# Kernel tuning notes

Measured on AMD Instinct MI355X. Metric: run time of the kernel, lower is better.

Reference implementation:

```python
import jax, jax.numpy as jnp
import numpy as np

B, L, C_IN = 32, 8192, 64
K, F = 3, 128


def setup_inputs() -> dict:
    key = jax.random.key(0)
    k1, k2 = jax.random.split(key)
    x = jax.random.normal(k1, (B, L, C_IN), dtype=jnp.float32)
    # glorot-ish scale for the conv kernel [k, C_in, F] (TF WIO layout)
    w = jax.random.normal(k2, (K, C_IN, F), dtype=jnp.float32) * (2.0 / (K * C_IN + F)) ** 0.5
    b = jnp.zeros((F,), dtype=jnp.float32)
    return {"x": x, "w": w, "b": b}


def reference(x, w, b):
    # Original: per-position matmul+trace == valid conv1d; then bias + relu.
    # x: [B, L, C_in], w: [K, C_in, F] -> out: [B, L-K+1, F]
    out = jax.lax.conv_general_dilated(
        x, w,
        window_strides=(1,),
        padding="VALID",
        dimension_numbers=("NWC", "WIO", "NWC"),
    )
    return jax.nn.relu(out + b)
```

## Files before the change

### kernel.cpp

```cpp
#include <hip/hip_runtime.h>
#include <hip/hip_bf16.h>

typedef __attribute__((ext_vector_type(8))) short short8;
typedef __attribute__((ext_vector_type(4))) float floatx4;

#define B_SZ   32
#define L_IN   8192
#define C_INCH 64
#define KW     3
#define F_OUT  128
#define L_OUT  (L_IN - KW + 1)
#define KDIM   (KW * C_INCH)

#define TILE_L  64
#define AROWS   (TILE_L + 2)
#define ASTRIDE 72
#define NGRID   (B_SZ * (L_IN / TILE_L))

#define WTAB_ELEMS (8 * 6 * 64)

__device__ __forceinline__ unsigned pk2(float a, float b) {
    __hip_bfloat162 h = __float22bfloat162_rn(make_float2(a, b));
    unsigned u;
    __builtin_memcpy(&u, &h, 4);
    return u;
}

__global__ __launch_bounds__(256) void w_prep(const float* __restrict__ w,
                                              short8* __restrict__ wtab) {
    int id = blockIdx.x * 256 + threadIdx.x;
    if (id >= WTAB_ELEMS) return;
    int lane = id & 63;
    int s    = (id >> 6) % 6;
    int nt   = id / 384;
    int nl = lane & 15, q = lane >> 4;
    const float* __restrict__ wf = w + nt * 16 + nl;
    float t[8];
#pragma unroll
    for (int j = 0; j < 8; ++j) t[j] = wf[(s * 32 + q * 8 + j) * F_OUT];
    union { unsigned u[4]; short8 v; } hb;
    hb.u[0] = pk2(t[0], t[1]);
    hb.u[1] = pk2(t[2], t[3]);
    hb.u[2] = pk2(t[4], t[5]);
    hb.u[3] = pk2(t[6], t[7]);
    wtab[id] = hb.v;
}

template <bool PREP>
__global__ __launch_bounds__(256, 4) void conv1d_mfma(const float* __restrict__ x,
                                                      const float* __restrict__ w,
                                                      const float* __restrict__ bias,
                                                      float* __restrict__ out,
                                                      const short8* __restrict__ wtab) {
    __shared__ short a_lds[AROWS * ASTRIDE];

    const int tid  = threadIdx.x;
    const int lane = tid & 63;
    const int wave = tid >> 6;
    const int q    = lane >> 4;
    const int nl   = lane & 15;

    const int g  = blockIdx.x;
    const int b  = g >> 7;
    const int l0 = (g & 127) * TILE_L;

    short8 bfrag[6][2];
    if (PREP) {
#pragma unroll
        for (int n = 0; n < 2; ++n)
#pragma unroll
            for (int s = 0; s < 6; ++s)
                bfrag[s][n] = wtab[(((wave * 2 + n) * 6 + s) << 6) + lane];
    } else {
#pragma unroll
        for (int n = 0; n < 2; ++n) {
            const int f = (wave * 2 + n) * 16 + nl;
            const float* __restrict__ wf = w + f;
#pragma unroll
            for (int s = 0; s < 6; ++s) {
                float t[8];
#pragma unroll
                for (int j = 0; j < 8; ++j)
                    t[j] = wf[(s * 32 + q * 8 + j) * F_OUT];
                union { unsigned u[4]; short8 v; } hb;
                hb.u[0] = pk2(t[0], t[1]);
                hb.u[1] = pk2(t[2], t[3]);
                hb.u[2] = pk2(t[4], t[5]);
                hb.u[3] = pk2(t[6], t[7]);
                bfrag[s][n] = hb.v;
            }
        }
    }

    float4 bv[2];
#pragma unroll
    for (int n = 0; n < 2; ++n)
        bv[n] = *(const float4*)(bias + (wave * 2 + n) * 16 + q * 4);

#pragma unroll
    for (int i = 0; i < 3; ++i) {
        int c = tid + 256 * i;
        if (c < AROWS * 8) {
            int p   = c >> 3;
            int col = (c & 7) * 8;
            int gl  = l0 + p;
            float4 v0, v1;
            if (gl < L_IN) {
                const float4* xp =
                    (const float4*)(x + ((size_t)b * L_IN + gl) * C_INCH + col);
                v0 = xp[0];
                v1 = xp[1];
            } else {
                v0 = make_float4(0.f, 0.f, 0.f, 0.f);
                v1 = v0;
            }
            union { unsigned u[4]; short8 v; } h;
            h.u[0] = pk2(v0.x, v0.y);
            h.u[1] = pk2(v0.z, v0.w);
            h.u[2] = pk2(v1.x, v1.y);
            h.u[3] = pk2(v1.z, v1.w);
            *(short8*)&a_lds[p * ASTRIDE + col] = h.v;
        }
    }
    __syncthreads();

    floatx4 acc[4][2];
#pragma unroll
    for (int m = 0; m < 4; ++m)
#pragma unroll
        for (int n = 0; n < 2; ++n) acc[m][n] = (floatx4){0.f, 0.f, 0.f, 0.f};

#pragma unroll
    for (int s = 0; s < 6; ++s) {
#pragma unroll
        for (int m = 0; m < 4; ++m) {
            short8 af = *(const short8*)&a_lds[(m * 16 + nl + (s >> 1)) * ASTRIDE
                                               + (s & 1) * 32 + q * 8];
#pragma unroll
            for (int n = 0; n < 2; ++n)
                acc[m][n] = __builtin_amdgcn_mfma_f32_16x16x32_bf16(
                    bfrag[s][n], af, acc[m][n], 0, 0, 0);
        }
    }

#pragma unroll
    for (int n = 0; n < 2; ++n) {
        const int fb = (wave * 2 + n) * 16 + q * 4;
#pragma unroll
        for (int m = 0; m < 4; ++m) {
            const int l = l0 + m * 16 + nl;
            if (l < L_OUT) {
                float4 v;
                v.x = acc[m][n][0] + bv[n].x;
                v.y = acc[m][n][1] + bv[n].y;
                v.z = acc[m][n][2] + bv[n].z;
                v.w = acc[m][n][3] + bv[n].w;
                v.x = v.x > 0.f ? v.x : 0.f;
                v.y = v.y > 0.f ? v.y : 0.f;
                v.z = v.z > 0.f ? v.z : 0.f;
                v.w = v.w > 0.f ? v.w : 0.f;
                *(float4*)(out + ((size_t)b * L_OUT + l) * F_OUT + fb) = v;
            }
        }
    }
}

extern "C" void kernel_launch(void* const* d_in, const int* in_sizes, int n_in,
                              void* d_out, int out_size, void* d_ws, size_t ws_size,
                              hipStream_t stream) {
    const float* x    = (const float*)d_in[0];
    const float* w    = (const float*)d_in[1];
    const float* bias = (const float*)d_in[2];
    float* out        = (float*)d_out;

    if (d_ws != nullptr && ws_size >= (size_t)WTAB_ELEMS * sizeof(short8)) {
        short8* wtab = (short8*)d_ws;
        w_prep<<<dim3((WTAB_ELEMS + 255) / 256), 256, 0, stream>>>(w, wtab);
        conv1d_mfma<true><<<dim3(NGRID), 256, 0, stream>>>(x, w, bias, out, wtab);
    } else {
        conv1d_mfma<false><<<dim3(NGRID), 256, 0, stream>>>(x, w, bias, out, nullptr);
    }
}
```

Baseline: 191.7 us.

## Process four tiles per block with async global-to-LDS prefetch of next tile

Each block now handles four consecutive 64-row tiles, so the grid shrinks by a factor of four. The raw fp32 input is staged into LDS with global_load_lds. The next tile's load is issued before the current tile's MFMA and store phase, so input fetch overlaps compute and output writes. A separate pass converts the staged fp32 data to bf16 in a second LDS buffer. This adds LDS footprint, hand-placed waitcnt/barrier synchronisation whose correctness depends on vmcnt ordering, and fewer blocks in flight.

```diff
diff --git a/kernel.cpp b/kernel.cpp
--- a/kernel.cpp
+++ b/kernel.cpp
@@ -15,7 +15,11 @@
 #define TILE_L  64
 #define AROWS   (TILE_L + 2)
 #define ASTRIDE 72
-#define NGRID   (B_SZ * (L_IN / TILE_L))
+#define TPB     4
+#define NGRID   (B_SZ * (L_IN / TILE_L) / TPB)
+
+#define XCHUNKS (AROWS * 16)
+#define BUNITS  (AROWS * 8)
 
 #define WTAB_ELEMS (8 * 6 * 64)
 
@@ -52,7 +56,8 @@
                                                       const float* __restrict__ bias,
                                                       float* __restrict__ out,
                                                       const short8* __restrict__ wtab) {
-    __shared__ short a_lds[AROWS * ASTRIDE];
+    __shared__ __align__(16) float a_raw[AROWS * C_INCH];
+    __shared__ __align__(16) short b_lds[AROWS * ASTRIDE];
 
     const int tid  = threadIdx.x;
     const int lane = tid & 63;
@@ -60,9 +65,9 @@
     const int q    = lane >> 4;
     const int nl   = lane & 15;
 
-    const int g  = blockIdx.x;
-    const int b  = g >> 7;
-    const int l0 = (g & 127) * TILE_L;
+    const int g      = blockIdx.x;
+    const int b      = g >> 5;
+    const int l_base = (g & 31) * (TPB * TILE_L);
 
     short8 bfrag[6][2];
     if (PREP) {
@@ -97,70 +102,98 @@
     for (int n = 0; n < 2; ++n)
         bv[n] = *(const float4*)(bias + (wave * 2 + n) * 16 + q * 4);
 
-#pragma unroll
-    for (int i = 0; i < 3; ++i) {
-        int c = tid + 256 * i;
-        if (c < AROWS * 8) {
-            int p   = c >> 3;
-            int col = (c & 7) * 8;
-            int gl  = l0 + p;
-            float4 v0, v1;
-            if (gl < L_IN) {
-                const float4* xp =
-                    (const float4*)(x + ((size_t)b * L_IN + gl) * C_INCH + col);
-                v0 = xp[0];
-                v1 = xp[1];
-            } else {
-                v0 = make_float4(0.f, 0.f, 0.f, 0.f);
-                v1 = v0;
-            }
-            union { unsigned u[4]; short8 v; } h;
-            h.u[0] = pk2(v0.x, v0.y);
-            h.u[1] = pk2(v0.z, v0.w);
-            h.u[2] = pk2(v1.x, v1.y);
-            h.u[3] = pk2(v1.z, v1.w);
-            *(short8*)&a_lds[p * ASTRIDE + col] = h.v;
-        }
-    }
+    auto stage = [&](int l0) {
+#pragma unroll
+        for (int r = 0; r < 5; ++r) {
+            int c = r * 256 + tid;
+            if (c < XCHUNKS) {
+                int row  = c >> 4;
+                int pc   = c & 15;
+                int grow = b * L_IN + l0 + row;
+                grow = grow < (B_SZ * L_IN - 1) ?
+                       grow : (B_SZ * L_IN - 1);
+                const float* src = x + (size_t)grow * C_INCH + pc * 4;
+                float* dst = &a_raw[(r * 256 + wave * 64) * 4];
+                __builtin_amdgcn_global_load_lds(
+                    (const __attribute__((address_space(1))) void*)src,
+                    (__attribute__((address_space(3))) void*)dst, 16, 0, 0);
+            }
+        }
+    };
+
+    stage(l_base);
     __syncthreads();
 
-    floatx4 acc[4][2];
-#pragma unroll
-    for (int m = 0; m < 4; ++m)
-#pragma unroll
-        for (int n = 0; n < 2; ++n) acc[m][n] = (floatx4){0.f, 0.f, 0.f, 0.f};
-
-#pragma unroll
-    for (int s = 0; s < 6; ++s) {
-#pragma unroll
-        for (int m = 0; m < 4; ++m) {
-            short8 af = *(const short8*)&a_lds[(m * 16 + nl + (s >> 1)) * ASTRIDE
-                                               + (s & 1) * 32 + q * 8];
-#pragma unroll
-            for (int n = 0; n < 2; ++n)
-                acc[m][n] = __builtin_amdgcn_mfma_f32_16x16x32_bf16(
-                    bfrag[s][n], af, acc[m][n], 0, 0, 0);
-        }
-    }
-
-#pragma unroll
-    for (int n = 0; n < 2; ++n) {
-        const int fb = (wave * 2 + n) * 16 + q * 4;
-#pragma unroll
-        for (int m = 0; m < 4; ++m) {
-            const int l = l0 + m * 16 + nl;
-            if (l < L_OUT) {
-                float4 v;
-                v.x = acc[m][n][0] + bv[n].x;
-                v.y = acc[m][n][1] + bv[n].y;
-                v.z = acc[m][n][2] + bv[n].z;
-                v.w = acc[m][n][3] + bv[n].w;
-                v.x = v.x > 0.f ? v.x : 0.f;
-                v.y = v.y > 0.f ? v.y : 0.f;
-                v.z = v.z > 0.f ? v.z : 0.f;
-                v.w = v.w > 0.f ? v.w : 0.f;
-                *(float4*)(out + ((size_t)b * L_OUT + l) * F_OUT + fb) = v;
-            }
+#pragma unroll
+    for (int t = 0; t < TPB; ++t) {
+        const int l0 = l_base + t * TILE_L;
+
+#pragma unroll
+        for (int r = 0; r < 3; ++r) {
+            int u = r * 256 + tid;
+            if (u < BUNITS) {
+                int p = u >> 3, cb = u & 7;
+                const floatx4* ap = (const floatx4*)&a_raw[p * C_INCH + cb * 8];
+                floatx4 a0 = ap[0], a1 = ap[1];
+                union { unsigned uu[4]; short8 v; } h;
+                h.uu[0] = pk2(a0[0], a0[1]);
+                h.uu[1] = pk2(a0[2], a0[3]);
+                h.uu[2] = pk2(a1[0], a1[1]);
+                h.uu[3] = pk2(a1[2], a1[3]);
+                *(short8*)&b_lds[p * ASTRIDE + cb * 8] = h.v;
+            }
+        }
+        asm volatile("s_waitcnt lgkmcnt(0)" ::: "memory");
+        __builtin_amdgcn_s_barrier();
+
+        if (t + 1 < TPB) {
+            stage(l0 + TILE_L);
+            __builtin_amdgcn_sched_barrier(0);
+        }
+
+        floatx4 acc[4][2];
+#pragma unroll
+        for (int m = 0; m < 4; ++m)
+#pragma unroll
+            for (int n = 0; n < 2; ++n) acc[m][n] = (floatx4){0.f, 0.f, 0.f, 0.f};
+
+#pragma unroll
+        for (int s = 0; s < 6; ++s) {
+#pragma unroll
+            for (int m = 0; m < 4; ++m) {
+                short8 af = *(const short8*)&b_lds[(m * 16 + nl + (s >> 1)) * ASTRIDE
+                                                   + (s & 1) * 32 + q * 8];
+#pragma unroll
+                for (int n = 0; n < 2; ++n)
+                    acc[m][n] = __builtin_amdgcn_mfma_f32_16x16x32_bf16(
+                        bfrag[s][n], af, acc[m][n], 0, 0, 0);
+            }
+        }
+
+#pragma unroll
+        for (int n = 0; n < 2; ++n) {
+            const int fb = (wave * 2 + n) * 16 + q * 4;
+#pragma unroll
+            for (int m = 0; m < 4; ++m) {
+                const int l = l0 + m * 16 + nl;
+                if (l < L_OUT) {
+                    float4 v;
+                    v.x = acc[m][n][0] + bv[n].x;
+                    v.y = acc[m][n][1] + bv[n].y;
+                    v.z = acc[m][n][2] + bv[n].z;
+                    v.w = acc[m][n][3] + bv[n].w;
+                    v.x = v.x > 0.f ? v.x : 0.f;
+                    v.y = v.y > 0.f ? v.y : 0.f;
+                    v.z = v.z > 0.f ? v.z : 0.f;
+                    v.w = v.w > 0.f ? v.w : 0.f;
+                    *(float4*)(out + ((size_t)b * L_OUT + l) * F_OUT + fb) = v;
+                }
+            }
+        }
+
+        if (t + 1 < TPB) {
+            asm volatile("s_waitcnt vmcnt(8)" ::: "memory");
+            __builtin_amdgcn_s_barrier();
         }
     }
 }
```

New measurement: 204.3 us. 1.07x slower.

## Load x tile directly to LDS as fp32 with XOR swizzle, convert at read

Applied to the files above, without the earlier changes.

The input tile is now copied from global memory straight into LDS with global_load_lds in fp32, skipping the register round-trip and the bf16 packing at load time. A per-row XOR swizzle on 16-byte chunks is meant to avoid LDS bank conflicts on the fragment reads. The bf16 conversion moves into the MFMA loop, so each element gets converted several times (rows are reused across the three taps). LDS use roughly doubles, which may limit occupancy, and out-of-range rows are clamped rather than zeroed.

```diff
diff --git a/kernel.cpp b/kernel.cpp
--- a/kernel.cpp
+++ b/kernel.cpp
@@ -14,8 +14,9 @@
 
 #define TILE_L  64
 #define AROWS   (TILE_L + 2)
-#define ASTRIDE 72
 #define NGRID   (B_SZ * (L_IN / TILE_L))
+
+#define XCHUNKS (AROWS * 16)
 
 #define WTAB_ELEMS (8 * 6 * 64)
 
@@ -52,7 +53,7 @@
                                                       const float* __restrict__ bias,
                                                       float* __restrict__ out,
                                                       const short8* __restrict__ wtab) {
-    __shared__ short a_lds[AROWS * ASTRIDE];
+    __shared__ __align__(16) float a_raw[AROWS * C_INCH];
 
     const int tid  = threadIdx.x;
     const int lane = tid & 63;
@@ -98,28 +99,20 @@
         bv[n] = *(const float4*)(bias + (wave * 2 + n) * 16 + q * 4);
 
 #pragma unroll
-    for (int i = 0; i < 3; ++i) {
-        int c = tid + 256 * i;
-        if (c < AROWS * 8) {
-            int p   = c >> 3;
-            int col = (c & 7) * 8;
-            int gl  = l0 + p;
-            float4 v0, v1;
-            if (gl < L_IN) {
-                const float4* xp =
-                    (const float4*)(x + ((size_t)b * L_IN + gl) * C_INCH + col);
-                v0 = xp[0];
-                v1 = xp[1];
-            } else {
-                v0 = make_float4(0.f, 0.f, 0.f, 0.f);
-                v1 = v0;
-            }
-            union { unsigned u[4]; short8 v; } h;
-            h.u[0] = pk2(v0.x, v0.y);
-            h.u[1] = pk2(v0.z, v0.w);
-            h.u[2] = pk2(v1.x, v1.y);
-            h.u[3] = pk2(v1.z, v1.w);
-            *(short8*)&a_lds[p * ASTRIDE + col] = h.v;
+    for (int r = 0; r < 5; ++r) {
+        int c = r * 256 + tid;
+        if (c < XCHUNKS) {
+            int row = c >> 4;
+            int pc  = c & 15;
+            int spc = pc ^ (row & 7);
+            int grow = b * L_IN + l0 + row;
+            grow = grow < (B_SZ * L_IN - 1) ?
+                   grow : (B_SZ * L_IN - 1);
+            const float* src = x + (size_t)grow * C_INCH + spc * 4;
+            float* dst = &a_raw[(r * 256 + wave * 64) * 4];
+            __builtin_amdgcn_global_load_lds(
+                (const __attribute__((address_space(1))) void*)src,
+                (__attribute__((address_space(3))) void*)dst, 16, 0, 0);
         }
     }
     __syncthreads();
@@ -134,12 +127,20 @@
     for (int s = 0; s < 6; ++s) {
 #pragma unroll
         for (int m = 0; m < 4; ++m) {
-            short8 af = *(const short8*)&a_lds[(m * 16 + nl + (s >> 1)) * ASTRIDE
-                                               + (s & 1) * 32 + q * 8];
+            const int row = m * 16 + nl + (s >> 1);
+            const int fxr = row & 7;
+            const int pc0 = (s & 1) * 8 + q * 2;
+            floatx4 c0 = *(const floatx4*)&a_raw[row * C_INCH + (pc0 ^ fxr) * 4];
+            floatx4 c1 = *(const floatx4*)&a_raw[row * C_INCH + ((pc0 + 1) ^ fxr) * 4];
+            union { unsigned u[4]; short8 v; } h;
+            h.u[0] = pk2(c0[0], c0[1]);
+            h.u[1] = pk2(c0[2], c0[3]);
+            h.u[2] = pk2(c1[0], c1[1]);
+            h.u[3] = pk2(c1[2], c1[3]);
 #pragma unroll
             for (int n = 0; n < 2; ++n)
                 acc[m][n] = __builtin_amdgcn_mfma_f32_16x16x32_bf16(
-                    bfrag[s][n], af, acc[m][n], 0, 0, 0);
+                    bfrag[s][n], h.v, acc[m][n], 0, 0, 0);
         }
     }
 
```

Measured after the change: 193.1 us. Within noise of the previous version (+0.7%).
